# Kernel optimization log

Hardware: AMD Instinct MI355X
Metric: run time of the kernel (lower is better)

The kernel has to match this reference:

```python
import jax, jax.numpy as jnp
import numpy as np

N, E, F, T = 10000, 160000, 4, 12   # nodes, edges, features, periods
C, HID, OUT = 512, 256, 12          # tgcn out_channels, head hidden, output_dim


def setup_inputs() -> dict:
    key = jax.random.key(0)
    ks = jax.random.split(key, 24)
    g = lambda k, s: (jax.random.normal(k, s, dtype=jnp.float32) * 0.05)
    inp = {
        "x": jax.random.normal(ks[0], (N, F, T), dtype=jnp.float32),
        "edge_index": jax.random.randint(ks[1], (2, E), 0, N, dtype=jnp.int32),
        "edge_attr": jax.random.uniform(ks[2], (E,), dtype=jnp.float32),
        "att": g(ks[3], (T,)),
        # TGCN gates: GCNConv (W [F,C], b [C]) + Linear on cat([conv, H]) ([2C,C], [C])
        "Wz_g": g(ks[4], (F, C)), "bz_g": jnp.zeros((C,), jnp.float32),
        "Wz_l": g(ks[5], (2 * C, C)), "bz_l": jnp.zeros((C,), jnp.float32),
        "Wr_g": g(ks[6], (F, C)), "br_g": jnp.zeros((C,), jnp.float32),
        "Wr_l": g(ks[7], (2 * C, C)), "br_l": jnp.zeros((C,), jnp.float32),
        "Wh_g": g(ks[8], (F, C)), "bh_g": jnp.zeros((C,), jnp.float32),
        "Wh_l": g(ks[9], (2 * C, C)), "bh_l": jnp.zeros((C,), jnp.float32),
        # dense head
        "W1": g(ks[10], (C, HID)), "b1": jnp.zeros((HID,), jnp.float32),
        "W2": g(ks[11], (HID, OUT)), "b2": jnp.zeros((OUT,), jnp.float32),
    }
    return inp


def reference(x, edge_index, edge_attr, att,
              Wz_g, bz_g, Wz_l, bz_l,
              Wr_g, br_g, Wr_l, br_l,
              Wh_g, bh_g, Wh_l, bh_l,
              W1, b1, W2, b2):
    n = x.shape[0]
    # GCN normalization with self loops (fill value 1.0), computed once
    loops = jnp.arange(n, dtype=edge_index.dtype)
    src = jnp.concatenate([edge_index[0], loops])
    dst = jnp.concatenate([edge_index[1], loops])
    w = jnp.concatenate([edge_attr, jnp.ones((n,), x.dtype)])
    deg = jax.ops.segment_sum(w, dst, num_segments=n)
    dinv = jax.lax.rsqrt(jnp.maximum(deg, 1e-12))
    norm = dinv[src] * w * dinv[dst]  # [E+N]

    def gcn(xt, W, b):
        xw = xt @ W                                   # [N,C]
        msg = norm[:, None] * xw[src]                 # gather over edges
        return jax.ops.segment_sum(msg, dst, num_segments=n) + b

    probs = jax.nn.softmax(att)            # attention over periods
    xt_seq = jnp.moveaxis(x, -1, 0)        # [T,N,F]
    H0 = jnp.zeros((n, C), x.dtype)

    def step(carry, inp):
        H, acc = carry
        xt, p = inp
        z = jax.nn.sigmoid(jnp.concatenate([gcn(xt, Wz_g, bz_g), H], axis=1) @ Wz_l + bz_l)
        r = jax.nn.sigmoid(jnp.concatenate([gcn(xt, Wr_g, br_g), H], axis=1) @ Wr_l + br_l)
        ht = jnp.tanh(jnp.concatenate([gcn(xt, Wh_g, bh_g), H * r], axis=1) @ Wh_l + bh_l)
        Hn = z * H + (1.0 - z) * ht
        return (Hn, acc + p * Hn), None

    (Hf, H_accum), _ = jax.lax.scan(step, (H0, H0), (xt_seq, probs))
    out_hidden = H_accum
    h = jax.nn.relu(H_accum)
    h = jax.nn.relu(h @ W1 + b1)
    h = h @ W2 + b2
    return (h, out_hidden)
```

## Files before the change

### kernel.cpp

```cpp
#include <hip/hip_runtime.h>
#include <math.h>

#define NF 48
#define TT 12

typedef __bf16 v8bf __attribute__((ext_vector_type(8)));
typedef float v16f __attribute__((ext_vector_type(16)));

__device__ __forceinline__ void gld16(const void* g, void* l) {
  __builtin_amdgcn_global_load_lds(
      (const __attribute__((address_space(1))) void*)(uintptr_t)g,
      (__attribute__((address_space(3))) void*)(uintptr_t)l, 16, 0, 0);
}


__global__ void k_init(float* __restrict__ deg, int* __restrict__ cnt, int n) {
  int i = blockIdx.x * blockDim.x + threadIdx.x;
  if (i < n) { deg[i] = 1.0f; cnt[i] = 0; cnt[n + i] = 0; }
}

__global__ void k_edge(const int* __restrict__ dst, const float* __restrict__ w,
                       float* __restrict__ deg, int* __restrict__ cnt, int e) {
  int i = blockIdx.x * blockDim.x + threadIdx.x;
  if (i < e) {
    int d = dst[i];
    atomicAdd(&deg[d], w[i]);
    atomicAdd(&cnt[d], 1);
  }
}


__global__ void k_scan1(const int* __restrict__ cnt, int* __restrict__ pscan,
                        int* __restrict__ bsum, const float* __restrict__ deg,
                        float* __restrict__ dinv, int n) {
  __shared__ int s[256];
  int i = blockIdx.x * 256 + threadIdx.x;
  int v = (i < n) ? cnt[i] : 0;
  s[threadIdx.x] = v;
  __syncthreads();
  for (int off = 1; off < 256; off <<= 1) {
    int t = 0;
    if (threadIdx.x >= off) t = s[threadIdx.x - off];
    __syncthreads();
    s[threadIdx.x] += t;
    __syncthreads();
  }
  if (i < n) {
    pscan[i] = s[threadIdx.x] - v;
    dinv[i] = rsqrtf(fmaxf(deg[i], 1e-12f));
  }
  if (threadIdx.x == 255) bsum[blockIdx.x] = s[255];
}

__global__ void k_scan2(const int* __restrict__ bsum, int* __restrict__ bpre, int nb,
                        const float* __restrict__ att, float* __restrict__ probs) {
  if (blockIdx.x == 0 && threadIdx.x == 0) {
    int run = 0;
    for (int b = 0; b < nb; b++) { bpre[b] = run; run += bsum[b]; }
  }
  if (blockIdx.x == 0 && threadIdx.x == 64) {
    float m = -1e30f;
    for (int t = 0; t < TT; t++) m = fmaxf(m, att[t]);
    float e[TT], s = 0.f;
    for (int t = 0; t < TT; t++) { e[t] = expf(att[t] - m); s += e[t]; }
    for (int t = 0; t < TT; t++) probs[t] = e[t] / s;
  }
}

__global__ void k_scan3(const int* __restrict__ pscan, const int* __restrict__ bpre,
                        int* __restrict__ offs, int n, int e) {
  int i = blockIdx.x * blockDim.x + threadIdx.x;
  if (i < n) offs[i] = pscan[i] + bpre[i >> 8];
  if (i == 0) offs[n] = e;
}

__global__ void k_place(const int* __restrict__ src, const int* __restrict__ dst,
                        const float* __restrict__ w, const int* __restrict__ offs,
                        int* __restrict__ fill, int* __restrict__ csrc,
                        float* __restrict__ cw, int e) {
  int i = blockIdx.x * blockDim.x + threadIdx.x;
  if (i >= e) return;
  int d = dst[i];
  int p = offs[d] + atomicAdd(&fill[d], 1);
  csrc[p] = src[i];
  cw[p] = w[i];
}

__global__ void k_gather(const int* __restrict__ offs, const int* __restrict__ csrc,
                         const float* __restrict__ cw, const float* __restrict__ dinv,
                         const float* __restrict__ x, float* __restrict__ Y, int n) {
  int tg = blockIdx.x * blockDim.x + threadIdx.x;
  if (tg >= n * 12) return;
  int i = tg / 12, q = tg % 12;
  float di = dinv[i];
  const float4* x4 = (const float4*)x;
  float4 sv = x4[(size_t)i * 12 + q];
  float ax = di * sv.x, ay = di * sv.y, az = di * sv.z, aw = di * sv.w;
  int e1 = offs[i + 1];
  for (int e = offs[i]; e < e1; e++) {
    int s = csrc[e];
    float wv = cw[e] * dinv[s];
    float4 xv = x4[(size_t)s * 12 + q];
    ax = fmaf(wv, xv.x, ax); ay = fmaf(wv, xv.y, ay);
    az = fmaf(wv, xv.z, az); aw = fmaf(wv, xv.w, aw);
  }
  float4 o = make_float4(di * ax, di * ay, di * az, di * aw);
  ((float4*)Y)[(size_t)i * 12 + q] = o;
}

__device__ __forceinline__ size_t packIdx128(int n, int k) {
  int row = n & 127;
  int c = (k & 31) >> 3;
  return (size_t)(n >> 7) * (128 * 512) + (size_t)(k >> 5) * (128 * 32) +
         (size_t)row * 32 + (size_t)((c ^ ((row >> 1) & 3)) << 3) + (k & 7);
}

__global__ void k_pack3(const float* __restrict__ Wzl, const float* __restrict__ Wrl,
                        const float* __restrict__ Whl, const float* __restrict__ W1,
                        __bf16* __restrict__ WzrP, __bf16* __restrict__ WhP,
                        __bf16* __restrict__ W1P) {
  __shared__ __bf16 t[64][72];
  int modew = blockIdx.z;
  if (modew == 1 && blockIdx.x >= 8) return;
  if (modew == 2 && blockIdx.x >= 4) return;
  int n0 = blockIdx.x * 64, k0 = blockIdx.y * 64;
  __bf16* WT = (modew == 0) ? WzrP : (modew == 1) ? WhP : W1P;
#pragma unroll
  for (int p = 0; p < 4; p++) {
    int kk = p * 16 + (threadIdx.x >> 4);
    int nn = (threadIdx.x & 15) * 4;
    int n = n0 + nn, k = k0 + kk;
    float4 v;
    if (modew == 2) {
      v = *(const float4*)(W1 + (size_t)k * 256 + n);
    } else {
      const float* src = (modew == 1) ? Whl : Wzl;
      int nc = n;
      if (modew == 0 && n >= 512) { src = Wrl; nc = n - 512; }
      v = *(const float4*)(src + (size_t)(512 + k) * 512 + nc);
    }
    t[kk][nn + 0] = (__bf16)v.x; t[kk][nn + 1] = (__bf16)v.y;
    t[kk][nn + 2] = (__bf16)v.z; t[kk][nn + 3] = (__bf16)v.w;
  }
  __syncthreads();
#pragma unroll
  for (int u = 0; u < 2; u++) {
    int unit = threadIdx.x * 2 + u;
    int nl = unit >> 3, kg = unit & 7;
    v8bf o;
#pragma unroll
    for (int j = 0; j < 8; j++) o[j] = t[kg * 8 + j][nl];
    *(v8bf*)(WT + packIdx128(n0 + nl, k0 + kg * 8)) = o;
  }
}

__global__ void k_build_eff3(const float* __restrict__ Wzg, const float* __restrict__ Wzl,
                             const float* __restrict__ bzg, const float* __restrict__ bzl,
                             const float* __restrict__ Wrg, const float* __restrict__ Wrl,
                             const float* __restrict__ brg, const float* __restrict__ brl,
                             const float* __restrict__ Whg, const float* __restrict__ Whl,
                             const float* __restrict__ bhg, const float* __restrict__ bhl,
                             float* __restrict__ WzrE, float* __restrict__ bzrE,
                             float* __restrict__ WhE, float* __restrict__ bhE) {
  int idx = blockIdx.x * blockDim.x + threadIdx.x;
  if (idx >= 3 * 5 * 512) return;
  int seg = idx / 2560;
  int r = (idx % 2560) / 512, c = idx % 512;
  const float *Wg, *Wl, *bg, *bl;
  float *We, *be;
  int ostride, ooff;
  if (seg == 0) { Wg = Wzg; Wl = Wzl; bg = bzg; bl = bzl; We = WzrE; be = bzrE; ostride = 1024; ooff = 0; }
  else if (seg == 1) { Wg = Wrg; Wl = Wrl; bg = brg; bl = brl; We = WzrE; be = bzrE; ostride = 1024; ooff = 512; }
  else { Wg = Whg; Wl = Whl; bg = bhg; bl = bhl; We = WhE; be = bhE; ostride = 512; ooff = 0; }
  float s = 0.f;
  if (r < 4) {
    for (int k = 0; k < 512; k++) s += Wg[r * 512 + k] * Wl[k * 512 + c];
    We[r * ostride + ooff + c] = s;
  } else {
    for (int k = 0; k < 512; k++) s += bg[k] * Wl[k * 512 + c];
    be[ooff + c] = s + bl[c];
  }
}

__global__ void k_wy3(const float* __restrict__ WzrE, const float* __restrict__ bzrE,
                      const float* __restrict__ WhE, const float* __restrict__ bhE,
                      const float* __restrict__ b1,
                      __bf16* __restrict__ WyZR, __bf16* __restrict__ WyH,
                      __bf16* __restrict__ Wy1) {
  int idx = blockIdx.x * blockDim.x + threadIdx.x;
  const float* Weff; const float* beff; __bf16* out; int Nout, loc;
  if (idx < 1024 * 16) { Weff = WzrE; beff = bzrE; out = WyZR; Nout = 1024; loc = idx; }
  else if (idx < (1024 + 512) * 16) { Weff = WhE; beff = bhE; out = WyH; Nout = 512; loc = idx - 1024 * 16; }
  else if (idx < (1024 + 512 + 256) * 16) { Weff = nullptr; beff = b1; out = Wy1; Nout = 256; loc = idx - (1024 + 512) * 16; }
  else return;
  int n = loc >> 4, k = loc & 15;
  float v = 0.f;
  if (k < 4) v = Weff ? Weff[k * Nout + n] : 0.f;
  else if (k == 4) v = beff[n];
  out[(size_t)(n >> 7) * 2048 + (size_t)(n & 127) * 16 + k] = (__bf16)v;
}

__global__ void k_yat0(const float* __restrict__ Y,
                       const float* __restrict__ WzrE, const float* __restrict__ bzrE,
                       const float* __restrict__ WhE, const float* __restrict__ bhE,
                       __bf16* __restrict__ Ya, __bf16* __restrict__ H1, int n) {
  int idx = blockIdx.x * blockDim.x + threadIdx.x;
  int nt0 = n * 512;
  if (idx < nt0) {
    int i = idx >> 9, c = idx & 511;
    float y0 = Y[(size_t)i * NF + 0], y1 = Y[(size_t)i * NF + 12];
    float y2 = Y[(size_t)i * NF + 24], y3 = Y[(size_t)i * NF + 36];
    float pz = bzrE[c] + y0 * WzrE[c] + y1 * WzrE[1024 + c] +
               y2 * WzrE[2048 + c] + y3 * WzrE[3072 + c];
    float ph = bhE[c] + y0 * WhE[c] + y1 * WhE[512 + c] +
               y2 * WhE[1024 + c] + y3 * WhE[1536 + c];
    float z = 1.f / (1.f + expf(-pz));
    H1[idx] = (__bf16)((1.f - z) * tanhf(ph));
  } else {
    int r = idx - nt0;
    if (r >= TT * n * 16) return;
    int t = r / (n * 16);
    int loc = r % (n * 16);
    int nn = loc >> 4, k = loc & 15;
    float v = 0.f;
    if (k < 4) v = Y[(size_t)nn * NF + k * TT + t];
    else if (k == 4) v = 1.f;
    Ya[r] = (__bf16)v;
  }
}

template <int MODE>
__global__ __launch_bounds__(256, 4) void k_mm(
    const __bf16* __restrict__ Agm, const __bf16* __restrict__ Bp,
    const __bf16* __restrict__ Hc, const __bf16* __restrict__ Zbf,
    const __bf16* __restrict__ Ay, const __bf16* __restrict__ Wy,
    float* __restrict__ Ofp, __bf16* __restrict__ Obf, __bf16* __restrict__ ObfR,
    int M, int RB) {
  constexpr int BUFS = 6144;
  __shared__ __bf16 smem[21504];

  const int RBX = (RB + 7) >> 3;
  {
    int xcd = blockIdx.x & 7;
    int idx = blockIdx.x >> 3;
    int rowblk = xcd * RBX + idx % RBX;
    int colblk = idx / RBX;
    if (rowblk >= RB) return;

    const int row0 = rowblk * 64;
    const int tid = threadIdx.x;
    const int lane = tid & 63, w = tid >> 6;
    const int wr = (w >> 1) * 32, wc = (w & 1) * 64;
    const int l31 = lane & 31, lh = lane >> 5;

    const int ar = tid >> 2, ac = tid & 3;
    const __bf16* At = Agm + (size_t)(row0 + ar) * 512 + ((ac ^ ((ar >> 1) & 3)) << 3);
    const __bf16* Bt = Bp + (size_t)colblk * (128 * 512);

    v16f acc[2];
#pragma unroll
    for (int j = 0; j < 2; j++)
#pragma unroll
      for (int q = 0; q < 16; q++) acc[j][q] = 0.f;

    auto stage = [&](int buf, int kt) {
      __bf16* base = smem + buf * BUFS;
      gld16(At + kt * 32, base + w * 512);
      const __bf16* bs = Bt + (size_t)kt * 4096 + (size_t)tid * 8;
      gld16(bs, base + 2048 + w * 512);
      gld16(bs + 2048, base + 4096 + w * 512);
    };
    auto stageY = [&]() {
      if (w < 2)
        gld16(Ay + (size_t)(row0 + (tid >> 1)) * 16 + (tid & 1) * 8,
              smem + 18432 + w * 512);
      gld16(Wy + (size_t)colblk * 2048 + (size_t)tid * 8, smem + 19456 + w * 512);
    };
    auto compute = [&](int buf) {
      const __bf16* base = smem + buf * BUFS;
      __builtin_amdgcn_s_setprio(1);
#pragma unroll
      for (int ks = 0; ks < 2; ks++) {
        int kc = ks * 2 + lh;
        int fr = wr + l31;
        v8bf a = *(const v8bf*)&base[fr * 32 + ((kc ^ ((fr >> 1) & 3)) << 3)];
#pragma unroll
        for (int ni = 0; ni < 2; ni++) {
          int fc = wc + ni * 32 + l31;
          v8bf b = *(const v8bf*)&base[2048 + fc * 32 + ((kc ^ ((fc >> 1) & 3)) << 3)];
          acc[ni] = __builtin_amdgcn_mfma_f32_32x32x16_bf16(a, b, acc[ni], 0, 0, 0);
        }
      }
      __builtin_amdgcn_s_setprio(0);
    };
    auto computeY = [&]() {
      const __bf16* ya = smem + 18432;
      const __bf16* yb = smem + 19456;
      v8bf a = *(const v8bf*)&ya[(wr + l31) * 16 + lh * 8];
#pragma unroll
      for (int ni = 0; ni < 2; ni++) {
        v8bf b = *(const v8bf*)&yb[(wc + ni * 32 + l31) * 16 + lh * 8];
        acc[ni] = __builtin_amdgcn_mfma_f32_32x32x16_bf16(a, b, acc[ni], 0, 0, 0);
      }
    };

    stageY();
    stage(0, 0);
    stage(1, 1);
#pragma unroll
    for (int kt = 0; kt < 16; kt++) {
      if (kt < 15)
        asm volatile("s_waitcnt vmcnt(3) lgkmcnt(0)\n\ts_barrier" ::: "memory");
      else
        asm volatile("s_waitcnt vmcnt(0) lgkmcnt(0)\n\ts_barrier" ::: "memory");
      if (kt < 14) stage((kt + 2) % 3, kt + 2);
      compute(kt % 3);
    }
    computeY();
    __syncthreads();

    if constexpr (MODE == 2) {
#pragma unroll
      for (int ni = 0; ni < 2; ni++) {
        int cl = wc + ni * 32 + l31;
#pragma unroll
        for (int reg = 0; reg < 16; reg++) {
          int rg = row0 + wr + (reg & 3) + ((reg >> 2) << 3) + (lh << 2);
          if (rg >= M) continue;
          Ofp[(size_t)rg * 256 + colblk * 128 + cl] = fmaxf(acc[ni][reg], 0.f);
        }
      }
    } else if constexpr (MODE == 0) {
#pragma unroll
      for (int ni = 0; ni < 2; ni++) {
        int cl = wc + ni * 32 + l31;
#pragma unroll
        for (int reg = 0; reg < 16; reg++) {
          int lr = wr + (reg & 3) + ((reg >> 2) << 3) + (lh << 2);
          smem[lr * 128 + cl] = (__bf16)(1.f / (1.f + expf(-acc[ni][reg])));
        }
      }
      __syncthreads();
      int row = tid >> 2, seg = (tid & 3) * 32;
      int rg = row0 + row;
      if (rg < M) {
        int cof = (colblk & 3) * 128;
        if (colblk < 4) {
#pragma unroll
          for (int q = 0; q < 4; q++) {
            uint4 v = *(const uint4*)&smem[row * 128 + seg + q * 8];
            *(uint4*)(Obf + (size_t)rg * 512 + cof + seg + q * 8) = v;
          }
        } else {
#pragma unroll
          for (int q = 0; q < 4; q++) {
            v8bf r8 = *(const v8bf*)&smem[row * 128 + seg + q * 8];
            v8bf h8 = *(const v8bf*)(Agm + (size_t)rg * 512 + cof + seg + q * 8);
            v8bf o;
#pragma unroll
            for (int j = 0; j < 8; j++) o[j] = (__bf16)((float)r8[j] * (float)h8[j]);
            *(v8bf*)(ObfR + (size_t)rg * 512 + cof + seg + q * 8) = o;
          }
        }
      }
    } else {
      float* sF = (float*)smem;
#pragma unroll
      for (int h = 0; h < 2; h++) {
        if ((w >> 1) == h) {
#pragma unroll
          for (int ni = 0; ni < 2; ni++) {
            int cl = wc + ni * 32 + l31;
#pragma unroll
            for (int reg = 0; reg < 16; reg++) {
              int lr = (reg & 3) + ((reg >> 2) << 3) + (lh << 2);
              sF[lr * 128 + cl] = tanhf(acc[ni][reg]);
            }
          }
        }
        __syncthreads();
        int row = tid >> 3, seg = (tid & 7) * 16;
        int rg = row0 + h * 32 + row;
        if (rg < M) {
          int cg0 = colblk * 128 + seg;
#pragma unroll
          for (int q = 0; q < 2; q++) {
            v8bf z8 = *(const v8bf*)(Zbf + (size_t)rg * 512 + cg0 + q * 8);
            v8bf h8 = *(const v8bf*)(Hc + (size_t)rg * 512 + cg0 + q * 8);
            v8bf o;
#pragma unroll
            for (int j = 0; j < 8; j++) {
              float z = (float)z8[j];
              float ht = sF[row * 128 + seg + q * 8 + j];
              o[j] = (__bf16)(z * (float)h8[j] + (1.f - z) * ht);
            }
            *(v8bf*)(Obf + (size_t)rg * 512 + cg0 + q * 8) = o;
          }
        }
        if (h == 0) __syncthreads();
      }
    }
  }
}

__global__ void k_acc(const __bf16* __restrict__ hist, const float* __restrict__ probs,
                      float* __restrict__ acc, __bf16* __restrict__ accRelu, int n) {
  int idx = blockIdx.x * blockDim.x + threadIdx.x;
  if (idx >= n * 64) return;
  size_t off = (size_t)idx * 8;
  size_t S = (size_t)n * 512;
  float s[8] = {0, 0, 0, 0, 0, 0, 0, 0};
#pragma unroll
  for (int t = 0; t < TT; t++) {
    float p = probs[t];
    v8bf h = *(const v8bf*)(hist + (size_t)(t + 1) * S + off);
#pragma unroll
    for (int j = 0; j < 8; j++) s[j] = fmaf(p, (float)h[j], s[j]);
  }
  *(float4*)(acc + off) = make_float4(s[0], s[1], s[2], s[3]);
  *(float4*)(acc + off + 4) = make_float4(s[4], s[5], s[6], s[7]);
  v8bf rl;
#pragma unroll
  for (int j = 0; j < 8; j++) rl[j] = (__bf16)fmaxf(s[j], 0.f);
  *(v8bf*)(accRelu + off) = rl;
}

__global__ void k_head2(const float* __restrict__ T1, const float* __restrict__ W2,
                        const float* __restrict__ b2, float* __restrict__ out0, int M) {
  int idx = blockIdx.x * blockDim.x + threadIdx.x;
  if (idx >= M * 12) return;
  int i = idx / 12, c = idx % 12;
  const float* tr = T1 + (size_t)i * 256;
  float s = b2[c];
  for (int k = 0; k < 256; k++) s = fmaf(tr[k], W2[k * 12 + c], s);
  out0[idx] = s;
}


extern "C" void kernel_launch(void* const* d_in, const int* in_sizes, int n_in,
                              void* d_out, int out_size, void* d_ws, size_t ws_size,
                              hipStream_t stream) {
  const float* x   = (const float*)d_in[0];
  const int*   ei  = (const int*)d_in[1];
  const float* ea  = (const float*)d_in[2];
  const float* att = (const float*)d_in[3];
  const float* Wzg = (const float*)d_in[4];  const float* bzg = (const float*)d_in[5];
  const float* Wzl = (const float*)d_in[6];  const float* bzl = (const float*)d_in[7];
  const float* Wrg = (const float*)d_in[8];  const float* brg = (const float*)d_in[9];
  const float* Wrl = (const float*)d_in[10]; const float* brl = (const float*)d_in[11];
  const float* Whg = (const float*)d_in[12]; const float* bhg = (const float*)d_in[13];
  const float* Whl = (const float*)d_in[14]; const float* bhl = (const float*)d_in[15];
  const float* W1  = (const float*)d_in[16]; const float* b1  = (const float*)d_in[17];
  const float* W2  = (const float*)d_in[18]; const float* b2  = (const float*)d_in[19];

  const int N = in_sizes[0] / NF;
  const int E = in_sizes[1] / 2;
  const int* srcI = ei;
  const int* dstI = ei + E;

  float* out0 = (float*)d_out;
  float* accO = (float*)d_out + (size_t)N * 12;

  char* wp = (char*)d_ws;
  auto carve = [&](size_t bytes) -> void* {
    void* p = (void*)wp;
    wp += (bytes + 255) & ~(size_t)255;
    return p;
  };
  float*  deg     = (float*)carve((size_t)N * 4);
  float*  dinv    = (float*)carve((size_t)N * 4);
  float*  probs   = (float*)carve(64);
  float*  Y       = (float*)carve((size_t)N * NF * 4);
  __bf16* WzrP    = (__bf16*)carve((size_t)1024 * 512 * 2);
  __bf16* WhP     = (__bf16*)carve((size_t)512 * 512 * 2);
  __bf16* W1P     = (__bf16*)carve((size_t)256 * 512 * 2);
  float*  Wzr_eff = (float*)carve((size_t)4 * 1024 * 4);
  float*  bzr_eff = (float*)carve((size_t)1024 * 4);
  float*  Wh_eff  = (float*)carve((size_t)4 * 512 * 4);
  float*  bh_eff  = (float*)carve((size_t)512 * 4);
  __bf16* hist    = (__bf16*)carve((size_t)(TT + 1) * N * 512 * 2);
  __bf16* Zbf     = (__bf16*)carve((size_t)N * 512 * 2);
  __bf16* Rbf     = (__bf16*)carve((size_t)N * 512 * 2);
  __bf16* accRelu = (__bf16*)carve((size_t)N * 512 * 2);
  float*  T1      = (float*)carve((size_t)N * 256 * 4);
  __bf16* Ya      = (__bf16*)carve((size_t)TT * N * 16 * 2);
  __bf16* WyZR    = (__bf16*)carve((size_t)1024 * 16 * 2);
  __bf16* WyH    = (__bf16*)carve((size_t)512 * 16 * 2);
  __bf16* Wy1     = (__bf16*)carve((size_t)256 * 16 * 2);
  int*    cnt     = (int*)carve((size_t)2 * N * 4);
  int*    fill    = cnt + N;
  int*    offs    = (int*)carve((size_t)(N + 1) * 4);
  int*    pscan   = (int*)carve((size_t)N * 4);
  int*    bsum    = (int*)carve(256);
  int*    bpre    = (int*)carve(256);
  int*    csrc    = (int*)carve((size_t)E * 4);
  float*  cw      = (float*)carve((size_t)E * 4);
  (void)carve(512 * 1024);
  (void)ws_size; (void)n_in; (void)out_size;

  const int TPB = 256;
  auto cdiv = [](int a, int b) { return (a + b - 1) / b; };
  const size_t S = (size_t)N * 512;

  k_init<<<cdiv(N, TPB), TPB, 0, stream>>>(deg, cnt, N);
  k_edge<<<cdiv(E, TPB), TPB, 0, stream>>>(dstI, ea, deg, cnt, E);

  const int nb = cdiv(N, 256);
  k_scan1<<<nb, 256, 0, stream>>>(cnt, pscan, bsum, deg, dinv, N);
  k_scan2<<<1, 128, 0, stream>>>(bsum, bpre, nb, att, probs);
  k_scan3<<<cdiv(N, TPB), TPB, 0, stream>>>(pscan, bpre, offs, N, E);
  k_place<<<cdiv(E, TPB), TPB, 0, stream>>>(srcI, dstI, ea, offs, fill, csrc, cw, E);
  k_gather<<<cdiv(N * 12, TPB), TPB, 0, stream>>>(offs, csrc, cw, dinv, x, Y, N);

  {
    dim3 gp(16, 8, 3);
    k_pack3<<<gp, 256, 0, stream>>>(Wzl, Wrl, Whl, W1, WzrP, WhP, W1P);
  }
  k_build_eff3<<<cdiv(3 * 5 * 512, TPB), TPB, 0, stream>>>(
      Wzg, Wzl, bzg, bzl, Wrg, Wrl, brg, brl, Whg, Whl, bhg, bhl,
      Wzr_eff, bzr_eff, Wh_eff, bh_eff);
  k_wy3<<<cdiv((1024 + 512 + 256) * 16, TPB), TPB, 0, stream>>>(
      Wzr_eff, bzr_eff, Wh_eff, bh_eff, b1, WyZR, WyH, Wy1);

  k_yat0<<<cdiv(N * 512 + TT * N * 16, TPB), TPB, 0, stream>>>(
      Y, Wzr_eff, bzr_eff, Wh_eff, bh_eff, Ya, hist + S, N);

  const int RB = cdiv(N, 64);
  const int RBX = cdiv(RB, 8);
  for (int t = 1; t < TT; t++) {
    const __bf16* Hbt = hist + (size_t)t * S;
    __bf16* Hbn = hist + (size_t)(t + 1) * S;
    const __bf16* Yat = Ya + (size_t)t * N * 16;
    k_mm<0><<<8 * RBX * 8, 256, 0, stream>>>(Hbt, WzrP, nullptr, nullptr, Yat, WyZR,
                                             nullptr, Zbf, Rbf, N, RB);
    k_mm<1><<<8 * RBX * 4, 256, 0, stream>>>(Rbf, WhP, Hbt, Zbf, Yat, WyH,
                                             nullptr, Hbn, nullptr, N, RB);
  }

  k_acc<<<cdiv(N * 64, TPB), TPB, 0, stream>>>(hist, probs, accO, accRelu, N);
  k_mm<2><<<8 * RBX * 2, 256, 0, stream>>>(accRelu, W1P, nullptr, nullptr, Ya, Wy1,
                                           T1, nullptr, nullptr, N, RB);
  k_head2<<<cdiv(N * 12, TPB), TPB, 0, stream>>>(T1, W2, b2, out0, N);
}
```

Before: 673.0 us.

## Fuse recurrent timestep GEMMs into persistent kernel with per-row-block dataflow counters

Replaces the 22 per-timestep k_mm launches for the gate and candidate GEMMs with one persistent kernel of 768 blocks. Each block loops over (timestep, row-block, column-block) work units. Global atomic counters per row block signal when the z/r tiles and the new-H tiles are done, so dependent work can start without a kernel boundary. This removes launch gaps and per-kernel tail idle time, and lets timesteps overlap across row blocks. In exchange it adds spin-waits and fences. It also relies on all 768 blocks being resident at once, otherwise it can deadlock.

After: 1.610 ms. +139.2%, slower.

```diff
diff --git a/kernel.cpp b/kernel.cpp
--- a/kernel.cpp
+++ b/kernel.cpp
@@ -229,6 +229,203 @@
   }
 }
 
+__device__ __forceinline__ void waitCtr(int* p, int target) {
+  if (threadIdx.x == 0) {
+    while (__hip_atomic_load(p, __ATOMIC_RELAXED, __HIP_MEMORY_SCOPE_SYSTEM) < target)
+      __builtin_amdgcn_s_sleep(2);
+    __builtin_amdgcn_fence(__ATOMIC_ACQUIRE, "agent");
+  }
+  __syncthreads();
+}
+__device__ __forceinline__ void postCtr(int* p) {
+  __syncthreads();
+  if (threadIdx.x == 0) {
+    __builtin_amdgcn_fence(__ATOMIC_RELEASE, "agent");
+    __hip_atomic_fetch_add(p, 1, __ATOMIC_RELAXED, __HIP_MEMORY_SCOPE_SYSTEM);
+  }
+}
+
+__device__ __forceinline__ void gemm64(
+    const int mode, const int row0, const int colblk,
+    const __bf16* __restrict__ Agm, const __bf16* __restrict__ Bp,
+    const __bf16* __restrict__ Hc, const __bf16* __restrict__ Zb,
+    const __bf16* __restrict__ Ay, const __bf16* __restrict__ Wy,
+    __bf16* __restrict__ Obf, __bf16* __restrict__ ObfR,
+    const int M, __bf16* smem) {
+  constexpr int BUFS = 6144;
+  const int tid = threadIdx.x;
+  const int lane = tid & 63, w = tid >> 6;
+  const int wr = (w >> 1) * 32, wc = (w & 1) * 64;
+  const int l31 = lane & 31, lh = lane >> 5;
+
+  const int ar = tid >> 2, ac = tid & 3;
+  const __bf16* At = Agm + (size_t)(row0 + ar) * 512 + ((ac ^ ((ar >> 1) & 3)) << 3);
+  const __bf16* Bt = Bp + (size_t)colblk * (128 * 512);
+
+  v16f acc[2];
+#pragma unroll
+  for (int j = 0; j < 2; j++)
+#pragma unroll
+    for (int q = 0; q < 16; q++) acc[j][q] = 0.f;
+
+  auto stage = [&](int buf, int kt) {
+    __bf16* base = smem + buf * BUFS;
+    gld16(At + kt * 32, base + w * 512);
+    const __bf16* bs = Bt + (size_t)kt * 4096 + (size_t)tid * 8;
+    gld16(bs, base + 2048 + w * 512);
+    gld16(bs + 2048, base + 4096 + w * 512);
+  };
+  auto stageY = [&]() {
+    if (w < 2)
+      gld16(Ay + (size_t)(row0 + (tid >> 1)) * 16 + (tid & 1) * 8,
+            smem + 18432 + w * 512);
+    gld16(Wy + (size_t)colblk * 2048 + (size_t)tid * 8, smem + 19456 + w * 512);
+  };
+  auto compute = [&](int buf) {
+    const __bf16* base = smem + buf * BUFS;
+    __builtin_amdgcn_s_setprio(1);
+#pragma unroll
+    for (int ks = 0; ks < 2; ks++) {
+      int kc = ks * 2 + lh;
+      int fr = wr + l31;
+      v8bf a = *(const v8bf*)&base[fr * 32 + ((kc ^ ((fr >> 1) & 3)) << 3)];
+#pragma unroll
+      for (int ni = 0; ni < 2; ni++) {
+        int fc = wc + ni * 32 + l31;
+        v8bf b = *(const v8bf*)&base[2048 + fc * 32 + ((kc ^ ((fc >> 1) & 3)) << 3)];
+        acc[ni] = __builtin_amdgcn_mfma_f32_32x32x16_bf16(a, b, acc[ni], 0, 0, 0);
+      }
+    }
+    __builtin_amdgcn_s_setprio(0);
+  };
+  auto computeY = [&]() {
+    const __bf16* ya = smem + 18432;
+    const __bf16* yb = smem + 19456;
+    v8bf a = *(const v8bf*)&ya[(wr + l31) * 16 + lh * 8];
+#pragma unroll
+    for (int ni = 0; ni < 2; ni++) {
+      v8bf b = *(const v8bf*)&yb[(wc + ni * 32 + l31) * 16 + lh * 8];
+      acc[ni] = __builtin_amdgcn_mfma_f32_32x32x16_bf16(a, b, acc[ni], 0, 0, 0);
+    }
+  };
+
+  stageY();
+  stage(0, 0);
+  stage(1, 1);
+#pragma unroll
+  for (int kt = 0; kt < 16; kt++) {
+    if (kt < 15)
+      asm volatile("s_waitcnt vmcnt(3) lgkmcnt(0)\n\ts_barrier" ::: "memory");
+    else
+      asm volatile("s_waitcnt vmcnt(0) lgkmcnt(0)\n\ts_barrier" ::: "memory");
+    if (kt < 14) stage((kt + 2) % 3, kt + 2);
+    compute(kt % 3);
+  }
+  computeY();
+  __syncthreads();
+
+  if (mode == 0) {
+#pragma unroll
+    for (int ni = 0; ni < 2; ni++) {
+      int cl = wc + ni * 32 + l31;
+#pragma unroll
+      for (int reg = 0; reg < 16; reg++) {
+        int lr = wr + (reg & 3) + ((reg >> 2) << 3) + (lh << 2);
+        smem[lr * 128 + cl] = (__bf16)(1.f / (1.f + expf(-acc[ni][reg])));
+      }
+    }
+    __syncthreads();
+    int row = tid >> 2, seg = (tid & 3) * 32;
+    int rg = row0 + row;
+    if (rg < M) {
+      int cof = (colblk & 3) * 128;
+      if (colblk < 4) {
+#pragma unroll
+        for (int q = 0; q < 4; q++) {
+          uint4 v = *(const uint4*)&smem[row * 128 + seg + q * 8];
+          *(uint4*)(Obf + (size_t)rg * 512 + cof + seg + q * 8) = v;
+        }
+      } else {
+#pragma unroll
+        for (int q = 0; q < 4; q++) {
+          v8bf r8 = *(const v8bf*)&smem[row * 128 + seg + q * 8];
+          v8bf h8 = *(const v8bf*)(Agm + (size_t)rg * 512 + cof + seg + q * 8);
+          v8bf o;
+#pragma unroll
+          for (int j = 0; j < 8; j++) o[j] = (__bf16)((float)r8[j] * (float)h8[j]);
+          *(v8bf*)(ObfR + (size_t)rg * 512 + cof + seg + q * 8) = o;
+        }
+      }
+    }
+  } else {
+    float* sF = (float*)smem;
+#pragma unroll
+    for (int h = 0; h < 2; h++) {
+      if ((w >> 1) == h) {
+#pragma unroll
+        for (int ni = 0; ni < 2; ni++) {
+          int cl = wc + ni * 32 + l31;
+#pragma unroll
+          for (int reg = 0; reg < 16; reg++) {
+            int lr = (reg & 3) + ((reg >> 2) << 3) + (lh << 2);
+            sF[lr * 128 + cl] = tanhf(acc[ni][reg]);
+          }
+        }
+      }
+      __syncthreads();
+      int row = tid >> 3, seg = (tid & 7) * 16;
+      int rg = row0 + h * 32 + row;
+      if (rg < M) {
+        int cg0 = colblk * 128 + seg;
+#pragma unroll
+        for (int q = 0; q < 2; q++) {
+          v8bf z8 = *(const v8bf*)(Zb + (size_t)rg * 512 + cg0 + q * 8);
+          v8bf h8 = *(const v8bf*)(Hc + (size_t)rg * 512 + cg0 + q * 8);
+          v8bf o;
+#pragma unroll
+          for (int j = 0; j < 8; j++) {
+            float z = (float)z8[j];
+            float ht = sF[row * 128 + seg + q * 8 + j];
+            o[j] = (__bf16)(z * (float)h8[j] + (1.f - z) * ht);
+          }
+          *(v8bf*)(Obf + (size_t)rg * 512 + cg0 + q * 8) = o;
+        }
+      }
+      if (h == 0) __syncthreads();
+    }
+  }
+}
+
+__global__ __launch_bounds__(256, 3) void k_tloop(
+    __bf16* __restrict__ hist, __bf16* __restrict__ Zbf, __bf16* __restrict__ Rbf,
+    const __bf16* __restrict__ WzrP, const __bf16* __restrict__ WhP,
+    const __bf16* __restrict__ WyZR, const __bf16* __restrict__ WyH,
+    const __bf16* __restrict__ Ya, int* __restrict__ ctr0, int* __restrict__ ctr1,
+    int M, int RB) {
+  __shared__ __bf16 smem[21504];
+  const size_t S = (size_t)M * 512;
+  const int J0 = RB * 8, JT = RB * 12;
+  for (int t = 1; t < TT; t++) {
+    const __bf16* Hbt = hist + (size_t)t * S;
+    __bf16* Hbn = hist + (size_t)(t + 1) * S;
+    const __bf16* Yat = Ya + (size_t)t * (size_t)M * 16;
+    for (int u = blockIdx.x; u < JT; u += gridDim.x) {
+      if (u < J0) {
+        int r = u >> 3, c = u & 7;
+        if (t > 1) waitCtr(&ctr1[(t - 1) * RB + r], 4);
+        gemm64(0, r * 64, c, Hbt, WzrP, nullptr, nullptr, Yat, WyZR, Zbf, Rbf, M, smem);
+        postCtr(&ctr0[t * RB + r]);
+      } else {
+        int v = u - J0;
+        int r = v >> 2, c = v & 3;
+        waitCtr(&ctr0[t * RB + r], 8);
+        gemm64(1, r * 64, c, Rbf, WhP, Hbt, Zbf, Yat, WyH, Hbn, nullptr, M, smem);
+        postCtr(&ctr1[t * RB + r]);
+      }
+    }
+  }
+}
+
 template <int MODE>
 __global__ __launch_bounds__(256, 4) void k_mm(
     const __bf16* __restrict__ Agm, const __bf16* __restrict__ Bp,
@@ -329,75 +526,6 @@
           if (rg >= M) continue;
           Ofp[(size_t)rg * 256 + colblk * 128 + cl] = fmaxf(acc[ni][reg], 0.f);
         }
-      }
-    } else if constexpr (MODE == 0) {
-#pragma unroll
-      for (int ni = 0; ni < 2; ni++) {
-        int cl = wc + ni * 32 + l31;
-#pragma unroll
-        for (int reg = 0; reg < 16; reg++) {
-          int lr = wr + (reg & 3) + ((reg >> 2) << 3) + (lh << 2);
-          smem[lr * 128 + cl] = (__bf16)(1.f / (1.f + expf(-acc[ni][reg])));
-        }
-      }
-      __syncthreads();
-      int row = tid >> 2, seg = (tid & 3) * 32;
-      int rg = row0 + row;
-      if (rg < M) {
-        int cof = (colblk & 3) * 128;
-        if (colblk < 4) {
-#pragma unroll
-          for (int q = 0; q < 4; q++) {
-            uint4 v = *(const uint4*)&smem[row * 128 + seg + q * 8];
-            *(uint4*)(Obf + (size_t)rg * 512 + cof + seg + q * 8) = v;
-          }
-        } else {
-#pragma unroll
-          for (int q = 0; q < 4; q++) {
-            v8bf r8 = *(const v8bf*)&smem[row * 128 + seg + q * 8];
-            v8bf h8 = *(const v8bf*)(Agm + (size_t)rg * 512 + cof + seg + q * 8);
-            v8bf o;
-#pragma unroll
-            for (int j = 0; j < 8; j++) o[j] = (__bf16)((float)r8[j] * (float)h8[j]);
-            *(v8bf*)(ObfR + (size_t)rg * 512 + cof + seg + q * 8) = o;
-          }
-        }
-      }
-    } else {
-      float* sF = (float*)smem;
-#pragma unroll
-      for (int h = 0; h < 2; h++) {
-        if ((w >> 1) == h) {
-#pragma unroll
-          for (int ni = 0; ni < 2; ni++) {
-            int cl = wc + ni * 32 + l31;
-#pragma unroll
-            for (int reg = 0; reg < 16; reg++) {
-              int lr = (reg & 3) + ((reg >> 2) << 3) + (lh << 2);
-              sF[lr * 128 + cl] = tanhf(acc[ni][reg]);
-            }
-          }
-        }
-        __syncthreads();
-        int row = tid >> 3, seg = (tid & 7) * 16;
-        int rg = row0 + h * 32 + row;
-        if (rg < M) {
-          int cg0 = colblk * 128 + seg;
-#pragma unroll
-          for (int q = 0; q < 2; q++) {
-            v8bf z8 = *(const v8bf*)(Zbf + (size_t)rg * 512 + cg0 + q * 8);
-            v8bf h8 = *(const v8bf*)(Hc + (size_t)rg * 512 + cg0 + q * 8);
-            v8bf o;
-#pragma unroll
-            for (int j = 0; j < 8; j++) {
-              float z = (float)z8[j];
-              float ht = sF[row * 128 + seg + q * 8 + j];
-              o[j] = (__bf16)(z * (float)h8[j] + (1.f - z) * ht);
-            }
-            *(v8bf*)(Obf + (size_t)rg * 512 + cg0 + q * 8) = o;
-          }
-        }
-        if (h == 0) __syncthreads();
       }
     }
   }
@@ -485,7 +613,7 @@
   float*  T1      = (float*)carve((size_t)N * 256 * 4);
   __bf16* Ya      = (__bf16*)carve((size_t)TT * N * 16 * 2);
   __bf16* WyZR    = (__bf16*)carve((size_t)1024 * 16 * 2);
-  __bf16* WyH    = (__bf16*)carve((size_t)512 * 16 * 2);
+  __bf16* WyH     = (__bf16*)carve((size_t)512 * 16 * 2);
   __bf16* Wy1     = (__bf16*)carve((size_t)256 * 16 * 2);
   int*    cnt     = (int*)carve((size_t)2 * N * 4);
   int*    fill    = cnt + N;
@@ -495,6 +623,9 @@
   int*    bpre    = (int*)carve(256);
   int*    csrc    = (int*)carve((size_t)E * 4);
   float*  cw      = (float*)carve((size_t)E * 4);
+  const int RB = (N + 63) / 64;
+  int*    ctr0    = (int*)carve((size_t)2 * 12 * RB * 4);
+  int*    ctr1    = ctr0 + 12 * RB;
   (void)carve(512 * 1024);
   (void)ws_size; (void)n_in; (void)out_size;
 
@@ -525,18 +656,11 @@
   k_yat0<<<cdiv(N * 512 + TT * N * 16, TPB), TPB, 0, stream>>>(
       Y, Wzr_eff, bzr_eff, Wh_eff, bh_eff, Ya, hist + S, N);
 
-  const int RB = cdiv(N, 64);
+  hipMemsetAsync(ctr0, 0, (size_t)2 * 12 * RB * 4, stream);
+  k_tloop<<<768, 256, 0, stream>>>(hist, Zbf, Rbf, WzrP, WhP, WyZR, WyH, Ya,
+                                   ctr0, ctr1, N, RB);
+
   const int RBX = cdiv(RB, 8);
-  for (int t = 1; t < TT; t++) {
-    const __bf16* Hbt = hist + (size_t)t * S;
-    __bf16* Hbn = hist + (size_t)(t + 1) * S;
-    const __bf16* Yat = Ya + (size_t)t * N * 16;
-    k_mm<0><<<8 * RBX * 8, 256, 0, stream>>>(Hbt, WzrP, nullptr, nullptr, Yat, WyZR,
-                                             nullptr, Zbf, Rbf, N, RB);
-    k_mm<1><<<8 * RBX * 4, 256, 0, stream>>>(Rbf, WhP, Hbt, Zbf, Yat, WyH,
-                                             nullptr, Hbn, nullptr, N, RB);
-  }
-
   k_acc<<<cdiv(N * 64, TPB), TPB, 0, stream>>>(hist, probs, accO, accRelu, N);
   k_mm<2><<<8 * RBX * 2, 256, 0, stream>>>(accRelu, W1P, nullptr, nullptr, Ya, Wy1,
                                            T1, nullptr, nullptr, N, RB);
```

## Fuse all GRU timesteps into one persistent kernel keeping H in LDS

Applied to the files above, without the earlier changes.

Replaces the per-timestep pair of GEMM launches (z/r gates, then candidate) with a single kernel where each 512-thread block owns 64 rows and loops over all timesteps. The hidden state stays resident in LDS, and z, r and the old H are kept in registers, so the Zbf/Rbf round trips through global memory and 22 launches are removed. The cost is only 157 blocks at one block per CU, which leaves part of the GPU idle. Every block also streams the full weight matrices from L2 each step, with less latency hiding than the earlier multi-block tiling.

New measurement: 1.510 ms. 124% more time.

```diff
diff --git a/kernel.cpp b/kernel.cpp
--- a/kernel.cpp
+++ b/kernel.cpp
@@ -229,175 +229,252 @@
   }
 }
 
-template <int MODE>
-__global__ __launch_bounds__(256, 4) void k_mm(
-    const __bf16* __restrict__ Agm, const __bf16* __restrict__ Bp,
-    const __bf16* __restrict__ Hc, const __bf16* __restrict__ Zbf,
-    const __bf16* __restrict__ Ay, const __bf16* __restrict__ Wy,
-    float* __restrict__ Ofp, __bf16* __restrict__ Obf, __bf16* __restrict__ ObfR,
-    int M, int RB) {
-  constexpr int BUFS = 6144;
-  __shared__ __bf16 smem[21504];
-
-  const int RBX = (RB + 7) >> 3;
-  {
-    int xcd = blockIdx.x & 7;
-    int idx = blockIdx.x >> 3;
-    int rowblk = xcd * RBX + idx % RBX;
-    int colblk = idx / RBX;
-    if (rowblk >= RB) return;
-
-    const int row0 = rowblk * 64;
-    const int tid = threadIdx.x;
-    const int lane = tid & 63, w = tid >> 6;
-    const int wr = (w >> 1) * 32, wc = (w & 1) * 64;
-    const int l31 = lane & 31, lh = lane >> 5;
-
-    const int ar = tid >> 2, ac = tid & 3;
-    const __bf16* At = Agm + (size_t)(row0 + ar) * 512 + ((ac ^ ((ar >> 1) & 3)) << 3);
-    const __bf16* Bt = Bp + (size_t)colblk * (128 * 512);
-
-    v16f acc[2];
-#pragma unroll
-    for (int j = 0; j < 2; j++)
-#pragma unroll
-      for (int q = 0; q < 16; q++) acc[j][q] = 0.f;
-
-    auto stage = [&](int buf, int kt) {
-      __bf16* base = smem + buf * BUFS;
-      gld16(At + kt * 32, base + w * 512);
-      const __bf16* bs = Bt + (size_t)kt * 4096 + (size_t)tid * 8;
-      gld16(bs, base + 2048 + w * 512);
-      gld16(bs + 2048, base + 4096 + w * 512);
+__global__ __launch_bounds__(512, 1) void k_gru(
+    const __bf16* __restrict__ H1, __bf16* __restrict__ hist,
+    const __bf16* __restrict__ WzrP, const __bf16* __restrict__ WhP,
+    const __bf16* __restrict__ WyZR, const __bf16* __restrict__ WyH,
+    const __bf16* __restrict__ Ya, int M) {
+  __shared__ __bf16 smem[62464];
+  constexpr int BOFF = 32768, WYOFF = 57344, AYOFF = 61440;
+  const int row0 = blockIdx.x * 64;
+  const int tid = threadIdx.x;
+  const int lane = tid & 63, w = tid >> 6;
+  const int h = w >> 2, q = w & 3;
+  const int l31 = lane & 31, lh = lane >> 5;
+  const size_t S = (size_t)M * 512;
+
+  auto gemmStrip = [&](const __bf16* Bpack, int p0, const __bf16* Wysrc, v16f* acc) {
+    gld16(Wysrc + (size_t)p0 * 2048 + (size_t)tid * 8, smem + WYOFF + w * 512);
+    auto stageB = [&](int buf, int kc) {
+      const __bf16* src = Bpack + (size_t)p0 * 65536 + (size_t)kc * 4096 + (size_t)tid * 8;
+      gld16(src, smem + BOFF + buf * 8192 + w * 512);
+      gld16(src + 65536, smem + BOFF + buf * 8192 + 4096 + w * 512);
     };
-    auto stageY = [&]() {
-      if (w < 2)
-        gld16(Ay + (size_t)(row0 + (tid >> 1)) * 16 + (tid & 1) * 8,
-              smem + 18432 + w * 512);
-      gld16(Wy + (size_t)colblk * 2048 + (size_t)tid * 8, smem + 19456 + w * 512);
-    };
-    auto compute = [&](int buf) {
-      const __bf16* base = smem + buf * BUFS;
+    stageB(0, 0);
+    stageB(1, 1);
+#pragma unroll
+    for (int kc = 0; kc < 16; kc++) {
+      if (kc < 15)
+        asm volatile("s_waitcnt vmcnt(2) lgkmcnt(0)\n\ts_barrier" ::: "memory");
+      else
+        asm volatile("s_waitcnt vmcnt(0) lgkmcnt(0)\n\ts_barrier" ::: "memory");
+      if (kc < 14) stageB((kc + 2) % 3, kc + 2);
+      const __bf16* B = smem + BOFF + (kc % 3) * 8192;
       __builtin_amdgcn_s_setprio(1);
 #pragma unroll
-      for (int ks = 0; ks < 2; ks++) {
-        int kc = ks * 2 + lh;
-        int fr = wr + l31;
-        v8bf a = *(const v8bf*)&base[fr * 32 + ((kc ^ ((fr >> 1) & 3)) << 3)];
+      for (int k16 = 0; k16 < 2; k16++) {
+        int row = h * 32 + l31;
+        int k8 = k16 * 2 + lh;
+        v8bf a = *(const v8bf*)&smem[row * 512 + kc * 32 +
+                                     ((k8 ^ ((row >> 1) & 3)) << 3)];
 #pragma unroll
         for (int ni = 0; ni < 2; ni++) {
-          int fc = wc + ni * 32 + l31;
-          v8bf b = *(const v8bf*)&base[2048 + fc * 32 + ((kc ^ ((fc >> 1) & 3)) << 3)];
+          int n = q * 64 + ni * 32 + l31;
+          v8bf b = *(const v8bf*)&B[n * 32 + ((k8 ^ ((n >> 1) & 3)) << 3)];
           acc[ni] = __builtin_amdgcn_mfma_f32_32x32x16_bf16(a, b, acc[ni], 0, 0, 0);
         }
       }
       __builtin_amdgcn_s_setprio(0);
-    };
-    auto computeY = [&]() {
-      const __bf16* ya = smem + 18432;
-      const __bf16* yb = smem + 19456;
-      v8bf a = *(const v8bf*)&ya[(wr + l31) * 16 + lh * 8];
+    }
+    {
+      v8bf a = *(const v8bf*)&smem[AYOFF + (h * 32 + l31) * 16 + lh * 8];
 #pragma unroll
       for (int ni = 0; ni < 2; ni++) {
-        v8bf b = *(const v8bf*)&yb[(wc + ni * 32 + l31) * 16 + lh * 8];
+        v8bf b = *(const v8bf*)&smem[WYOFF + (q * 64 + ni * 32 + l31) * 16 + lh * 8];
         acc[ni] = __builtin_amdgcn_mfma_f32_32x32x16_bf16(a, b, acc[ni], 0, 0, 0);
       }
-    };
-
-    stageY();
-    stage(0, 0);
-    stage(1, 1);
-#pragma unroll
-    for (int kt = 0; kt < 16; kt++) {
-      if (kt < 15)
-        asm volatile("s_waitcnt vmcnt(3) lgkmcnt(0)\n\ts_barrier" ::: "memory");
-      else
-        asm volatile("s_waitcnt vmcnt(0) lgkmcnt(0)\n\ts_barrier" ::: "memory");
-      if (kt < 14) stage((kt + 2) % 3, kt + 2);
-      compute(kt % 3);
-    }
-    computeY();
+    }
     __syncthreads();
-
-    if constexpr (MODE == 2) {
+  };
+
+#pragma unroll
+  for (int j = 0; j < 8; j++) {
+    int grp = tid + j * 512;
+    int row = grp >> 6, gp = grp & 63;
+    int gl = (gp & ~3) | ((gp & 3) ^ ((row >> 1) & 3));
+    gld16(H1 + (size_t)(row0 + row) * 512 + (size_t)gl * 8,
+          smem + ((size_t)j * 512 + (size_t)w * 64) * 8);
+  }
+  asm volatile("s_waitcnt vmcnt(0)" ::: "memory");
+  __syncthreads();
+
+  v8bf zpk[2][2][2], rpk[2][2][2], hpk[2][2][2];
+
+  for (int t = 1; t < TT; t++) {
+    if (tid < 128)
+      gld16(Ya + ((size_t)t * M + row0) * 16 + (size_t)tid * 8, smem + AYOFF + w * 512);
+
+#pragma unroll
+    for (int s = 0; s < 4; s++) {
+      v16f acc[2];
+#pragma unroll
+      for (int ni = 0; ni < 2; ni++)
+#pragma unroll
+        for (int r2 = 0; r2 < 16; r2++) acc[ni][r2] = 0.f;
+      gemmStrip(WzrP, 2 * s, WyZR, acc);
+#pragma unroll
+      for (int ni = 0; ni < 2; ni++)
+#pragma unroll
+        for (int reg = 0; reg < 16; reg++) {
+          float v = 1.f / (1.f + expf(-acc[ni][reg]));
+          if (s < 2) zpk[s][ni][reg >> 3][reg & 7] = (__bf16)v;
+          else rpk[s - 2][ni][reg >> 3][reg & 7] = (__bf16)v;
+        }
+    }
+
+#pragma unroll
+    for (int sp = 0; sp < 2; sp++)
 #pragma unroll
       for (int ni = 0; ni < 2; ni++) {
-        int cl = wc + ni * 32 + l31;
+        int col = sp * 256 + q * 64 + ni * 32 + l31;
+        int cb = (col >> 5) << 5, c3 = (col >> 3) & 3, c7 = col & 7;
 #pragma unroll
         for (int reg = 0; reg < 16; reg++) {
-          int rg = row0 + wr + (reg & 3) + ((reg >> 2) << 3) + (lh << 2);
-          if (rg >= M) continue;
-          Ofp[(size_t)rg * 256 + colblk * 128 + cl] = fmaxf(acc[ni][reg], 0.f);
+          int row = h * 32 + (reg & 3) + ((reg >> 2) << 3) + (lh << 2);
+          int ad = row * 512 + cb + ((c3 ^ ((row >> 1) & 3)) << 3) + c7;
+          float hv = (float)smem[ad];
+          hpk[sp][ni][reg >> 3][reg & 7] = (__bf16)hv;
+          smem[ad] = (__bf16)((float)rpk[sp][ni][reg >> 3][reg & 7] * hv);
         }
       }
-    } else if constexpr (MODE == 0) {
+    __syncthreads();
+
+    v16f acch[2][2];
+#pragma unroll
+    for (int sp = 0; sp < 2; sp++)
+#pragma unroll
+      for (int ni = 0; ni < 2; ni++)
+#pragma unroll
+        for (int r2 = 0; r2 < 16; r2++) acch[sp][ni][r2] = 0.f;
+#pragma unroll
+    for (int s = 0; s < 2; s++) gemmStrip(WhP, 2 * s, WyH, acch[s]);
+
+#pragma unroll
+    for (int sp = 0; sp < 2; sp++)
 #pragma unroll
       for (int ni = 0; ni < 2; ni++) {
-        int cl = wc + ni * 32 + l31;
+        int col = sp * 256 + q * 64 + ni * 32 + l31;
+        int cb = (col >> 5) << 5, c3 = (col >> 3) & 3, c7 = col & 7;
 #pragma unroll
         for (int reg = 0; reg < 16; reg++) {
-          int lr = wr + (reg & 3) + ((reg >> 2) << 3) + (lh << 2);
-          smem[lr * 128 + cl] = (__bf16)(1.f / (1.f + expf(-acc[ni][reg])));
+          int row = h * 32 + (reg & 3) + ((reg >> 2) << 3) + (lh << 2);
+          float ht = tanhf(acch[sp][ni][reg]);
+          float z = (float)zpk[sp][ni][reg >> 3][reg & 7];
+          float hs = (float)hpk[sp][ni][reg >> 3][reg & 7];
+          int ad = row * 512 + cb + ((c3 ^ ((row >> 1) & 3)) << 3) + c7;
+          smem[ad] = (__bf16)(z * hs + (1.f - z) * ht);
         }
       }
-      __syncthreads();
-      int row = tid >> 2, seg = (tid & 3) * 32;
+    __syncthreads();
+
+    __bf16* Hn = hist + (size_t)(t + 1) * S;
+#pragma unroll
+    for (int j = 0; j < 8; j++) {
+      int grp = tid + j * 512;
+      int row = grp >> 6, gp = grp & 63;
       int rg = row0 + row;
-      if (rg < M) {
-        int cof = (colblk & 3) * 128;
-        if (colblk < 4) {
-#pragma unroll
-          for (int q = 0; q < 4; q++) {
-            uint4 v = *(const uint4*)&smem[row * 128 + seg + q * 8];
-            *(uint4*)(Obf + (size_t)rg * 512 + cof + seg + q * 8) = v;
-          }
-        } else {
-#pragma unroll
-          for (int q = 0; q < 4; q++) {
-            v8bf r8 = *(const v8bf*)&smem[row * 128 + seg + q * 8];
-            v8bf h8 = *(const v8bf*)(Agm + (size_t)rg * 512 + cof + seg + q * 8);
-            v8bf o;
-#pragma unroll
-            for (int j = 0; j < 8; j++) o[j] = (__bf16)((float)r8[j] * (float)h8[j]);
-            *(v8bf*)(ObfR + (size_t)rg * 512 + cof + seg + q * 8) = o;
-          }
-        }
+      int ad = row * 512 + (gp & ~3) * 8 + (((gp & 3) ^ ((row >> 1) & 3)) << 3);
+      uint4 vv = *(const uint4*)&smem[ad];
+      if (rg < M) *(uint4*)(Hn + (size_t)rg * 512 + (size_t)gp * 8) = vv;
+    }
+  }
+}
+
+template <int MODE>
+__global__ __launch_bounds__(256, 4) void k_mm(
+    const __bf16* __restrict__ Agm, const __bf16* __restrict__ Bp,
+    const __bf16* __restrict__ Ay, const __bf16* __restrict__ Wy,
+    float* __restrict__ Ofp, int M, int RB) {
+  constexpr int BUFS = 6144;
+  __shared__ __bf16 smem[21504];
+
+  const int RBX = (RB + 7) >> 3;
+  int xcd = blockIdx.x & 7;
+  int idx = blockIdx.x >> 3;
+  int rowblk = xcd * RBX + idx % RBX;
+  int colblk = idx / RBX;
+  if (rowblk >= RB) return;
+
+  const int row0 = rowblk * 64;
+  const int tid = threadIdx.x;
+  const int lane = tid & 63, w = tid >> 6;
+  const int wr = (w >> 1) * 32, wc = (w & 1) * 64;
+  const int l31 = lane & 31, lh = lane >> 5;
+
+  const int ar = tid >> 2, ac = tid & 3;
+  const __bf16* At = Agm + (size_t)(row0 + ar) * 512 + ((ac ^ ((ar >> 1) & 3)) << 3);
+  const __bf16* Bt = Bp + (size_t)colblk * (128 * 512);
+
+  v16f acc[2];
+#pragma unroll
+  for (int j = 0; j < 2; j++)
+#pragma unroll
+    for (int p = 0; p < 16; p++) acc[j][p] = 0.f;
+
+  auto stage = [&](int buf, int kt) {
+    __bf16* base = smem + buf * BUFS;
+    gld16(At + kt * 32, base + w * 512);
+    const __bf16* bs = Bt + (size_t)kt * 4096 + (size_t)tid * 8;
+    gld16(bs, base + 2048 + w * 512);
+    gld16(bs + 2048, base + 4096 + w * 512);
+  };
+  auto stageY = [&]() {
+    if (w < 2)
+      gld16(Ay + (size_t)(row0 + (tid >> 1)) * 16 + (tid & 1) * 8,
+            smem + 18432 + w * 512);
+    gld16(Wy + (size_t)colblk * 2048 + (size_t)tid * 8, smem + 19456 + w * 512);
+  };
+  auto compute = [&](int buf) {
+    const __bf16* base = smem + buf * BUFS;
+    __builtin_amdgcn_s_setprio(1);
+#pragma unroll
+    for (int ks = 0; ks < 2; ks++) {
+      int kc = ks * 2 + lh;
+      int fr = wr + l31;
+      v8bf a = *(const v8bf*)&base[fr * 32 + ((kc ^ ((fr >> 1) & 3)) << 3)];
+#pragma unroll
+      for (int ni = 0; ni < 2; ni++) {
+        int fc = wc + ni * 32 + l31;
+        v8bf b = *(const v8bf*)&base[2048 + fc * 32 + ((kc ^ ((fc >> 1) & 3)) << 3)];
+        acc[ni] = __builtin_amdgcn_mfma_f32_32x32x16_bf16(a, b, acc[ni], 0, 0, 0);
       }
-    } else {
-      float* sF = (float*)smem;
-#pragma unroll
-      for (int h = 0; h < 2; h++) {
-        if ((w >> 1) == h) {
-#pragma unroll
-          for (int ni = 0; ni < 2; ni++) {
-            int cl = wc + ni * 32 + l31;
-#pragma unroll
-            for (int reg = 0; reg < 16; reg++) {
-              int lr = (reg & 3) + ((reg >> 2) << 3) + (lh << 2);
-              sF[lr * 128 + cl] = tanhf(acc[ni][reg]);
-            }
-          }
-        }
-        __syncthreads();
-        int row = tid >> 3, seg = (tid & 7) * 16;
-        int rg = row0 + h * 32 + row;
-        if (rg < M) {
-          int cg0 = colblk * 128 + seg;
-#pragma unroll
-          for (int q = 0; q < 2; q++) {
-            v8bf z8 = *(const v8bf*)(Zbf + (size_t)rg * 512 + cg0 + q * 8);
-            v8bf h8 = *(const v8bf*)(Hc + (size_t)rg * 512 + cg0 + q * 8);
-            v8bf o;
-#pragma unroll
-            for (int j = 0; j < 8; j++) {
-              float z = (float)z8[j];
-              float ht = sF[row * 128 + seg + q * 8 + j];
-              o[j] = (__bf16)(z * (float)h8[j] + (1.f - z) * ht);
-            }
-            *(v8bf*)(Obf + (size_t)rg * 512 + cg0 + q * 8) = o;
-          }
-        }
-        if (h == 0) __syncthreads();
+    }
+    __builtin_amdgcn_s_setprio(0);
+  };
+
+  stageY();
+  stage(0, 0);
+  stage(1, 1);
+#pragma unroll
+  for (int kt = 0; kt < 16; kt++) {
+    if (kt < 15)
+      asm volatile("s_waitcnt vmcnt(3) lgkmcnt(0)\n\ts_barrier" ::: "memory");
+    else
+      asm volatile("s_waitcnt vmcnt(0) lgkmcnt(0)\n\ts_barrier" ::: "memory");
+    if (kt < 14) stage((kt + 2) % 3, kt + 2);
+    compute(kt % 3);
+  }
+  {
+    const __bf16* ya = smem + 18432;
+    const __bf16* yb = smem + 19456;
+    v8bf a = *(const v8bf*)&ya[(wr + l31) * 16 + lh * 8];
+#pragma unroll
+    for (int ni = 0; ni < 2; ni++) {
+      v8bf b = *(const v8bf*)&yb[(wc + ni * 32 + l31) * 16 + lh * 8];
+      acc[ni] = __builtin_amdgcn_mfma_f32_32x32x16_bf16(a, b, acc[ni], 0, 0, 0);
+    }
+  }
+  __syncthreads();
+
+  if constexpr (MODE == 2) {
+#pragma unroll
+    for (int ni = 0; ni < 2; ni++) {
+      int cl = wc + ni * 32 + l31;
+#pragma unroll
+      for (int reg = 0; reg < 16; reg++) {
+        int rg = row0 + wr + (reg & 3) + ((reg >> 2) << 3) + (lh << 2);
+        if (rg >= M) continue;
+        Ofp[(size_t)rg * 256 + colblk * 128 + cl] = fmaxf(acc[ni][reg], 0.f);
       }
     }
   }
@@ -479,13 +556,11 @@
   float*  Wh_eff  = (float*)carve((size_t)4 * 512 * 4);
   float*  bh_eff  = (float*)carve((size_t)512 * 4);
   __bf16* hist    = (__bf16*)carve((size_t)(TT + 1) * N * 512 * 2);
-  __bf16* Zbf     = (__bf16*)carve((size_t)N * 512 * 2);
-  __bf16* Rbf     = (__bf16*)carve((size_t)N * 512 * 2);
   __bf16* accRelu = (__bf16*)carve((size_t)N * 512 * 2);
   float*  T1      = (float*)carve((size_t)N * 256 * 4);
   __bf16* Ya      = (__bf16*)carve((size_t)TT * N * 16 * 2);
   __bf16* WyZR    = (__bf16*)carve((size_t)1024 * 16 * 2);
-  __bf16* WyH    = (__bf16*)carve((size_t)512 * 16 * 2);
+  __bf16* WyH     = (__bf16*)carve((size_t)512 * 16 * 2);
   __bf16* Wy1     = (__bf16*)carve((size_t)256 * 16 * 2);
   int*    cnt     = (int*)carve((size_t)2 * N * 4);
   int*    fill    = cnt + N;
@@ -526,19 +601,10 @@
       Y, Wzr_eff, bzr_eff, Wh_eff, bh_eff, Ya, hist + S, N);
 
   const int RB = cdiv(N, 64);
+  k_gru<<<RB, 512, 0, stream>>>(hist + S, hist, WzrP, WhP, WyZR, WyH, Ya, N);
+
   const int RBX = cdiv(RB, 8);
-  for (int t = 1; t < TT; t++) {
-    const __bf16* Hbt = hist + (size_t)t * S;
-    __bf16* Hbn = hist + (size_t)(t + 1) * S;
-    const __bf16* Yat = Ya + (size_t)t * N * 16;
-    k_mm<0><<<8 * RBX * 8, 256, 0, stream>>>(Hbt, WzrP, nullptr, nullptr, Yat, WyZR,
-                                             nullptr, Zbf, Rbf, N, RB);
-    k_mm<1><<<8 * RBX * 4, 256, 0, stream>>>(Rbf, WhP, Hbt, Zbf, Yat, WyH,
-                                             nullptr, Hbn, nullptr, N, RB);
-  }
-
   k_acc<<<cdiv(N * 64, TPB), TPB, 0, stream>>>(hist, probs, accO, accRelu, N);
-  k_mm<2><<<8 * RBX * 2, 256, 0, stream>>>(accRelu, W1P, nullptr, nullptr, Ya, Wy1,
-                                           T1, nullptr, nullptr, N, RB);
+  k_mm<2><<<8 * RBX * 2, 256, 0, stream>>>(accRelu, W1P, Ya, Wy1, T1, N, RB);
   k_head2<<<cdiv(N * 12, TPB), TPB, 0, stream>>>(T1, W2, b2, out0, N);
 }
```
